# Kernel tuning notes

Measured on AMD Instinct MI355X. Metric: run time of the kernel, lower is better.

Reference implementation:

```python
import jax, jax.numpy as jnp
import numpy as np

# --- Mamba2Simple hyperparams (derived from init_kwargs) ---
D_MODEL = 2048
D_STATE = 128
HEADDIM = 64
EXPAND = 2
D_CONV = 4
NGROUPS = 1
CHUNK = 256
EPS = 1e-5
D_INNER = EXPAND * D_MODEL            # 4096
NHEADS = D_INNER // HEADDIM           # 64
CONV_DIM = D_INNER + 2 * NGROUPS * D_STATE          # 4352
D_IN_PROJ = 2 * D_INNER + 2 * NGROUPS * D_STATE + NHEADS  # 8512


def setup_inputs() -> dict:
    key = jax.random.key(0)
    ks = jax.random.split(key, 9)
    B, L = 2, 2048
    x = jax.random.normal(ks[0], (B, L, D_MODEL), jnp.float32)
    w_in = jax.random.normal(ks[1], (D_MODEL, D_IN_PROJ), jnp.float32) * (D_MODEL ** -0.5)
    conv_w = jax.random.normal(ks[2], (CONV_DIM, D_CONV), jnp.float32) * 0.2
    conv_b = jnp.zeros((CONV_DIM,), jnp.float32)
    dt_bias = jax.random.uniform(ks[3], (NHEADS,), jnp.float32, -4.0, -1.0)
    # A in [1, 16] per official init -> A_log = log(A)
    A_log = jnp.log(jax.random.uniform(ks[4], (NHEADS,), jnp.float32, 1.0, 16.0))
    D = jnp.ones((NHEADS,), jnp.float32)
    norm_w = jnp.ones((D_INNER,), jnp.float32)
    w_out = jax.random.normal(ks[5], (D_INNER, D_MODEL), jnp.float32) * (D_INNER ** -0.5)
    return {"x": x, "w_in": w_in, "conv_w": conv_w, "conv_b": conv_b,
            "dt_bias": dt_bias, "A_log": A_log, "D": D, "norm_w": norm_w, "w_out": w_out}


def _segsum(a):
    # a: (..., T) -> (..., T, T) with out[i, j] = sum_{k=j+1..i} a[k] for j<=i else -inf
    T = a.shape[-1]
    cs = jnp.cumsum(a, axis=-1)
    d = cs[..., :, None] - cs[..., None, :]
    mask = jnp.tril(jnp.ones((T, T), dtype=bool))
    return jnp.where(mask, d, -jnp.inf)


def _ssd(X, A, Bm, Cm):
    # X: (b, l, h, p) already multiplied by dt; A: (b, l, h) = dt*A_cont
    # Bm, Cm: (b, l, n)  (ngroups=1, broadcast over heads)
    b, l, h, p = X.shape
    n = Bm.shape[-1]
    c = l // CHUNK
    X = X.reshape(b, c, CHUNK, h, p)
    A = A.reshape(b, c, CHUNK, h).transpose(0, 3, 1, 2)      # (b, h, c, q)
    Bm = Bm.reshape(b, c, CHUNK, n)
    Cm = Cm.reshape(b, c, CHUNK, n)
    A_cs = jnp.cumsum(A, axis=-1)                             # (b, h, c, q)
    Lmat = jnp.exp(_segsum(A))                                # (b, h, c, q, q)
    # intra-chunk (diagonal block) output
    Y_diag = jnp.einsum("bcln,bcsn,bhcls,bcshp->bclhp", Cm, Bm, Lmat, X)
    # per-chunk final states
    decay_states = jnp.exp(A_cs[..., -1:] - A_cs)             # (b, h, c, q)
    states = jnp.einsum("bcln,bhcl,bclhp->bchpn", Bm, decay_states, X)
    # inter-chunk recurrence
    A_last = jnp.pad(A_cs[..., -1], ((0, 0), (0, 0), (1, 0)))  # (b, h, c+1)
    decay_chunk = jnp.exp(_segsum(A_last))                     # (b, h, c+1, c+1)
    states = jnp.concatenate([jnp.zeros_like(states[:, :1]), states], axis=1)
    states = jnp.einsum("bhzc,bchpn->bzhpn", decay_chunk, states)[:, :-1]
    # state -> output contribution
    Y_off = jnp.einsum("bchpn,bcln,bhcl->bclhp", states, Cm, jnp.exp(A_cs))
    return (Y_diag + Y_off).reshape(b, l, h, p)


def _mamba2(x, w_in, conv_w, conv_b, dt_bias, A_log, D, norm_w, w_out):
    B, L, _ = x.shape
    zxbcdt = jnp.einsum("bld,de->ble", x, w_in)               # (B, L, 8512)
    z = zxbcdt[..., :D_INNER]
    xBC = zxbcdt[..., D_INNER:D_INNER + CONV_DIM]
    dt = zxbcdt[..., D_INNER + CONV_DIM:]                      # (B, L, H)
    dt = jax.nn.softplus(dt + dt_bias)
    # causal depthwise conv1d + silu
    xp = jnp.pad(xBC, ((0, 0), (D_CONV - 1, 0), (0, 0)))
    acc = conv_b
    xBC = sum(conv_w[:, k] * xp[:, k:k + L, :] for k in range(D_CONV)) + conv_b
    xBC = jax.nn.silu(xBC)
    xh = xBC[..., :D_INNER].reshape(B, L, NHEADS, HEADDIM)
    Bm = xBC[..., D_INNER:D_INNER + NGROUPS * D_STATE]         # (B, L, N) since ngroups=1
    Cm = xBC[..., D_INNER + NGROUPS * D_STATE:]                # (B, L, N)
    A = -jnp.exp(A_log)                                        # (H,)
    y = _ssd(xh * dt[..., None], dt * A, Bm, Cm)               # (B, L, H, P)
    y = y + xh * D[None, None, :, None]                        # skip term
    y = y.reshape(B, L, D_INNER)
    # gated RMSNorm (norm_before_gate=False): normalize(y * silu(z)) * weight
    y = y * jax.nn.silu(z)
    y = y * jax.lax.rsqrt(jnp.mean(y * y, axis=-1, keepdims=True) + EPS) * norm_w
    return jnp.einsum("ble,ed->bld", y, w_out)


def reference(x, w_in, conv_w, conv_b, dt_bias, A_log, D, norm_w, w_out):
    return x + _mamba2(x, w_in, conv_w, conv_b, dt_bias, A_log, D, norm_w, w_out)
```

## Files before the change

### kernel.cpp

```cpp
#include <hip/hip_runtime.h>
#include <math.h>

#define DEV __device__ __forceinline__

typedef __attribute__((ext_vector_type(4))) float f32x4;
typedef __attribute__((ext_vector_type(4))) unsigned short u16x4;
typedef __attribute__((ext_vector_type(8))) unsigned short u16x8;
typedef __attribute__((ext_vector_type(8))) __bf16 bfv8;

DEV unsigned short f2bf(float f) {
  unsigned u = __builtin_bit_cast(unsigned, f);
  u = (u + 0x7FFFu + ((u >> 16) & 1u)) >> 16;
  return (unsigned short)u;
}
DEV float bf2f(unsigned short h) {
  unsigned u = ((unsigned)h) << 16;
  return __builtin_bit_cast(float, u);
}

DEV f32x4 mfma16(u16x8 a, u16x8 b, f32x4 c) {
  return __builtin_amdgcn_mfma_f32_16x16x32_bf16(
      __builtin_bit_cast(bfv8, a), __builtin_bit_cast(bfv8, b), c, 0, 0, 0);
}

DEV void gload_lds16(const unsigned short* g, unsigned short* s) {
  __builtin_amdgcn_global_load_lds(
      (const __attribute__((address_space(1))) void*)g,
      (__attribute__((address_space(3))) void*)s, 16, 0, 0);
}

template <int N>
DEV void vmcnt_wait() {
  if constexpr (N == 0) asm volatile("s_waitcnt vmcnt(0)" ::: "memory");
  else if constexpr (N == 2) asm volatile("s_waitcnt vmcnt(2)" ::: "memory");
  else if constexpr (N == 4) asm volatile("s_waitcnt vmcnt(4)" ::: "memory");
}

__global__ __launch_bounds__(512, 2) void gemm8_in(
    const unsigned short* __restrict__ A, const unsigned short* __restrict__ Bt,
    unsigned short* __restrict__ o_z, unsigned short* __restrict__ o_xbc,
    float* __restrict__ o_dt) {
  constexpr int K = 2048, NT = K / 64;
  __shared__ __align__(16) unsigned short As[2][256 * 64];
  __shared__ __align__(16) unsigned short Bs[2][256 * 64];
  const int tid = threadIdx.x;
  const int lane = tid & 63, w = tid >> 6;
  const int l16 = lane & 15, lq = lane >> 4;
  const int wr = w >> 1, wc = w & 1;
  const int nwg = gridDim.x * gridDim.y;
  int lin = blockIdx.y * gridDim.x + blockIdx.x;
  lin = (lin & 7) * (nwg >> 3) + (lin >> 3);
  const int m0 = (lin / gridDim.x) * 256, n0 = (lin % gridDim.x) * 256;
  const int srow = lane >> 3;
  const int schk = (lane & 7) ^ srow;
  const unsigned short* Ag = A + (size_t)(m0 + srow) * K + schk * 8;
  const unsigned short* Bg = Bt + (size_t)(n0 + srow) * K + schk * 8;
  const int px0 = lq ^ (l16 & 7);
  const int px1 = (4 + lq) ^ (l16 & 7);

  f32x4 acc[4][8] = {};

  auto stageA = [&](int p, int slot, int kt) {
    gload_lds16(Ag + (size_t)(slot * 64 + w * 8) * K + kt * 64,
                &As[p][(slot * 64 + w * 8) * 64]);
  };
  auto stageB = [&](int p, int slot, int kt) {
    gload_lds16(Bg + (size_t)(slot * 64 + w * 8) * K + kt * 64,
                &Bs[p][(slot * 64 + w * 8) * 64]);
  };
  auto rdA = [&](int p, int mf, int k2) -> u16x8 {
    const int row = wr * 64 + mf * 16 + l16;
    return *(const u16x8*)(&As[p][row * 64 + (k2 ? px1 : px0) * 8]);
  };
  auto rdB = [&](int p, int nf, int k2) -> u16x8 {
    const int row = wc * 128 + nf * 16 + l16;
    return *(const u16x8*)(&Bs[p][row * 64 + (k2 ? px1 : px0) * 8]);
  };

  stageA(0, 0, 0); stageA(0, 1, 0); stageA(0, 2, 0); stageA(0, 3, 0);
  stageB(0, 0, 0); stageB(0, 2, 0); stageB(0, 1, 0); stageB(0, 3, 0);
  vmcnt_wait<2>();
  __builtin_amdgcn_s_barrier();

  u16x8 a0[4], a1[4], b0[2], b1[2];
  for (int k = 0; k < NT; ++k) {
    const int p = k & 1, pn = p ^ 1;
    const bool st = (k + 1 < NT);
#pragma unroll
    for (int mf = 0; mf < 4; ++mf) { a0[mf] = rdA(p, mf, 0); a1[mf] = rdA(p, mf, 1); }
    b0[0] = rdB(p, 0, 0); b1[0] = rdB(p, 0, 1);
    b0[1] = rdB(p, 1, 0); b1[1] = rdB(p, 1, 1);
    if (st) { stageA(pn, 0, k + 1); stageA(pn, 1, k + 1); }
    __builtin_amdgcn_s_barrier();
    __builtin_amdgcn_s_setprio(1);
#pragma unroll
    for (int nf = 0; nf < 2; ++nf)
#pragma unroll
      for (int mf = 0; mf < 4; ++mf) {
        acc[mf][nf] = mfma16(a0[mf], b0[nf], acc[mf][nf]);
        acc[mf][nf] = mfma16(a1[mf], b1[nf], acc[mf][nf]);
      }
    __builtin_amdgcn_s_setprio(0);
    __builtin_amdgcn_s_barrier();
    b0[0] = rdB(p, 2, 0); b1[0] = rdB(p, 2, 1);
    b0[1] = rdB(p, 3, 0); b1[1] = rdB(p, 3, 1);
    if (st) { stageA(pn, 2, k + 1); stageA(pn, 3, k + 1); vmcnt_wait<4>(); }
    else vmcnt_wait<0>();
    __builtin_amdgcn_s_barrier();
    __builtin_amdgcn_s_setprio(1);
#pragma unroll
    for (int nf = 0; nf < 2; ++nf)
#pragma unroll
      for (int mf = 0; mf < 4; ++mf) {
        acc[mf][2 + nf] = mfma16(a0[mf], b0[nf], acc[mf][2 + nf]);
        acc[mf][2 + nf] = mfma16(a1[mf], b1[nf], acc[mf][2 + nf]);
      }
    __builtin_amdgcn_s_setprio(0);
    __builtin_amdgcn_s_barrier();
    b0[0] = rdB(p, 4, 0); b1[0] = rdB(p, 4, 1);
    b0[1] = rdB(p, 5, 0); b1[1] = rdB(p, 5, 1);
    if (st) { stageB(pn, 0, k + 1); stageB(pn, 2, k + 1); }
    __builtin_amdgcn_s_barrier();
    __builtin_amdgcn_s_setprio(1);
#pragma unroll
    for (int nf = 0; nf < 2; ++nf)
#pragma unroll
      for (int mf = 0; mf < 4; ++mf) {
        acc[mf][4 + nf] = mfma16(a0[mf], b0[nf], acc[mf][4 + nf]);
        acc[mf][4 + nf] = mfma16(a1[mf], b1[nf], acc[mf][4 + nf]);
      }
    __builtin_amdgcn_s_setprio(0);
    __builtin_amdgcn_s_barrier();
    b0[0] = rdB(p, 6, 0); b1[0] = rdB(p, 6, 1);
    b0[1] = rdB(p, 7, 0); b1[1] = rdB(p, 7, 1);
    if (st) { stageB(pn, 1, k + 1); stageB(pn, 3, k + 1); vmcnt_wait<2>(); }
    else vmcnt_wait<0>();
    __builtin_amdgcn_s_barrier();
    __builtin_amdgcn_s_setprio(1);
#pragma unroll
    for (int nf = 0; nf < 2; ++nf)
#pragma unroll
      for (int mf = 0; mf < 4; ++mf) {
        acc[mf][6 + nf] = mfma16(a0[mf], b0[nf], acc[mf][6 + nf]);
        acc[mf][6 + nf] = mfma16(a1[mf], b1[nf], acc[mf][6 + nf]);
      }
    __builtin_amdgcn_s_setprio(0);
    __builtin_amdgcn_s_barrier();
  }

#pragma unroll
  for (int mf = 0; mf < 4; ++mf) {
#pragma unroll
    for (int nf = 0; nf < 8; ++nf) {
      const int col = n0 + wc * 128 + nf * 16 + l16;
#pragma unroll
      for (int r = 0; r < 4; ++r) {
        const int row = m0 + wr * 64 + mf * 16 + lq * 4 + r;
        float v = acc[mf][nf][r];
        if (col < 4096) o_z[(size_t)row * 4096 + col] = f2bf(v);
        else if (col < 8448) o_xbc[(size_t)row * 4352 + (col - 4096)] = f2bf(v);
        else if (col < 8512) o_dt[(size_t)row * 64 + (col - 8448)] = v;
      }
    }
  }
}

__global__ __launch_bounds__(256, 3) void gemm_p(
    const unsigned short* __restrict__ A, const unsigned short* __restrict__ Bt,
    int K, float* __restrict__ o_c, const float* __restrict__ resid) {
  __shared__ __align__(16) unsigned short As[3][128 * 32];
  __shared__ __align__(16) unsigned short Bs[3][128 * 32];
  const int tid = threadIdx.x;
  const int lane = tid & 63, w = tid >> 6;
  const int l16 = lane & 15, lq = lane >> 4;
  const int wr = w >> 1, wc = w & 1;
  const int nwg = gridDim.x * gridDim.y;
  int lin = blockIdx.y * gridDim.x + blockIdx.x;
  lin = (lin & 7) * (nwg >> 3) + (lin >> 3);
  const int m0 = (lin / gridDim.x) * 128, n0 = (lin % gridDim.x) * 128;
  const int lrow = lane >> 2;
  const int gq = (lane & 3) ^ ((lrow >> 1) & 3);
  const int cq = lq ^ ((l16 >> 1) & 3);

  const unsigned short* Ag = A + (size_t)(m0 + lrow) * K + gq * 8;
  const unsigned short* Bg = Bt + (size_t)(n0 + lrow) * K + gq * 8;

  f32x4 acc[4][4] = {};

  auto stage = [&](int bi, int kt) {
#pragma unroll
    for (int i = 0; i < 2; ++i) {
      const int rb = (w + i * 4) * 16;
      gload_lds16(Ag + (size_t)rb * K + kt * 32, &As[bi][rb * 32]);
    }
#pragma unroll
    for (int i = 0; i < 2; ++i) {
      const int rb = (w + i * 4) * 16;
      gload_lds16(Bg + (size_t)rb * K + kt * 32, &Bs[bi][rb * 32]);
    }
  };

  const int nt = K / 32;
  stage(0, 0);
  stage(1, 1);

  for (int k = 0; k < nt; ++k) {
    const int cb = k % 3;
    if (k < nt - 1) vmcnt_wait<4>();
    else vmcnt_wait<0>();
    __builtin_amdgcn_s_barrier();
    if (k + 2 < nt) stage((k + 2) % 3, k + 2);

    u16x8 af[4], bf[4];
#pragma unroll
    for (int mf = 0; mf < 4; ++mf)
      af[mf] = *(const u16x8*)(&As[cb][(wr * 64 + mf * 16 + l16) * 32 + cq * 8]);
#pragma unroll
    for (int nf = 0; nf < 4; ++nf)
      bf[nf] = *(const u16x8*)(&Bs[cb][(wc * 64 + nf * 16 + l16) * 32 + cq * 8]);

    __builtin_amdgcn_s_setprio(1);
#pragma unroll
    for (int mf = 0; mf < 4; ++mf)
#pragma unroll
      for (int nf = 0; nf < 4; ++nf)
        acc[mf][nf] = mfma16(af[mf], bf[nf], acc[mf][nf]);
    __builtin_amdgcn_s_setprio(0);
  }

#pragma unroll
  for (int mf = 0; mf < 4; ++mf) {
#pragma unroll
    for (int nf = 0; nf < 4; ++nf) {
      const int col = n0 + wc * 64 + nf * 16 + l16;
#pragma unroll
      for (int r = 0; r < 4; ++r) {
        const int row = m0 + wr * 64 + mf * 16 + lq * 4 + r;
        size_t idx = (size_t)row * 2048 + col;
        o_c[idx] = acc[mf][nf][r] + resid[idx];
      }
    }
  }
}

__global__ __launch_bounds__(256) void convert_bf16(
    const float* __restrict__ in, unsigned short* __restrict__ out) {
  const size_t i = ((size_t)blockIdx.x * 256 + threadIdx.x) * 8;
  f32x4 a = *(const f32x4*)(in + i);
  f32x4 b = *(const f32x4*)(in + i + 4);
  u16x8 o;
#pragma unroll
  for (int j = 0; j < 4; ++j) { o[j] = f2bf(a[j]); o[j + 4] = f2bf(b[j]); }
  *(u16x8*)(out + i) = o;
}

__global__ __launch_bounds__(256) void transpose_conv(
    const float* __restrict__ in, unsigned short* __restrict__ out, int R,
    int C) {
  __shared__ __align__(16) unsigned short T[64][72];
  const int c0 = blockIdx.x * 64, r0 = blockIdx.y * 64;
  const int tid = threadIdx.x;
#pragma unroll
  for (int it = 0; it < 4; ++it) {
    int r = it * 16 + (tid >> 4);
    int c = (tid & 15) * 4;
    f32x4 v = {0.f, 0.f, 0.f, 0.f};
    if (c0 + c < C) v = *(const f32x4*)(in + (size_t)(r0 + r) * C + c0 + c);
#pragma unroll
    for (int j = 0; j < 4; ++j) T[c + j][r] = f2bf(v[j]);
  }
  __syncthreads();
  const int nr = tid >> 2, kc = (tid & 3) * 16;
  u16x8 a = *(const u16x8*)(&T[nr][kc]);
  u16x8 b = *(const u16x8*)(&T[nr][kc + 8]);
  unsigned short* o = out + (size_t)(c0 + nr) * R + r0 + kc;
  *(u16x8*)o = a;
  *(u16x8*)(o + 8) = b;
}

__global__ __launch_bounds__(256) void conv_kernel(
    const unsigned short* __restrict__ raw, const float* __restrict__ cw,
    const float* __restrict__ cb, unsigned short* __restrict__ xbc) {
  const int ch4 = blockIdx.x * 256 + threadIdx.x;
  if (ch4 >= 1088) return;
  const int ch = ch4 * 4;
  const int r0 = blockIdx.y * 4;
  const int l0 = r0 & 2047;
  f32x4 w0 = *(const f32x4*)(cw + ch * 4);
  f32x4 w1 = *(const f32x4*)(cw + ch * 4 + 4);
  f32x4 w2 = *(const f32x4*)(cw + ch * 4 + 8);
  f32x4 w3 = *(const f32x4*)(cw + ch * 4 + 12);
  f32x4 bias = *(const f32x4*)(cb + ch);
  f32x4 v[7];
#pragma unroll
  for (int i = 0; i < 7; ++i) {
    if (l0 - 3 + i >= 0) {
      u16x4 h = *(const u16x4*)(raw + (size_t)(r0 - 3 + i) * 4352 + ch);
      v[i] = (f32x4){bf2f(h[0]), bf2f(h[1]), bf2f(h[2]), bf2f(h[3])};
    } else {
      v[i] = (f32x4){0.f, 0.f, 0.f, 0.f};
    }
  }
#pragma unroll
  for (int j = 0; j < 4; ++j) {
    f32x4 acc = bias;
#pragma unroll
    for (int k = 0; k < 4; ++k) {
      acc[0] += w0[k] * v[j + k][0];
      acc[1] += w1[k] * v[j + k][1];
      acc[2] += w2[k] * v[j + k][2];
      acc[3] += w3[k] * v[j + k][3];
    }
    u16x4 o;
#pragma unroll
    for (int q = 0; q < 4; ++q) {
      float s = acc[q] / (1.0f + __expf(-acc[q]));
      o[q] = f2bf(s);
    }
    *(u16x4*)(xbc + (size_t)(r0 + j) * 4352 + ch) = o;
  }
}

__global__ __launch_bounds__(256) void dt_kernel(
    float* __restrict__ dtb, const float* __restrict__ dt_bias,
    const float* __restrict__ A_log, float* __restrict__ Acs) {
  __shared__ float ws[4];
  const int blk = blockIdx.x;
  const int c = blk & 7, h = (blk >> 3) & 63, b = blk >> 9;
  const int t = threadIdx.x;
  const int lane = t & 63, w = t >> 6;
  const int row = b * 2048 + c * 256 + t;
  float xv = dtb[(size_t)row * 64 + h] + dt_bias[h];
  float dt = (xv > 20.0f) ? xv : log1pf(__expf(xv));
  dtb[(size_t)row * 64 + h] = dt;
  float s = dt * (-__expf(A_log[h]));
#pragma unroll
  for (int off = 1; off < 64; off <<= 1) {
    float v = __shfl_up(s, off, 64);
    if (lane >= off) s += v;
  }
  if (lane == 63) ws[w] = s;
  __syncthreads();
  float base = 0.0f;
#pragma unroll
  for (int i = 0; i < 4; ++i)
    if (i < w) base += ws[i];
  Acs[((size_t)((b * 64 + h) * 8 + c)) * 256 + t] = s + base;
}

__global__ __launch_bounds__(256) void g_kernel(
    const unsigned short* __restrict__ xbc, float* __restrict__ G) {
  const int bc = blockIdx.y;
  const int i0 = (blockIdx.x >> 2) * 64, j0 = (blockIdx.x & 3) * 64;
  const int tid = threadIdx.x;
  const int lane = tid & 63, w = tid >> 6;
  const int l16 = lane & 15, lq = lane >> 4;
  const unsigned short* base = xbc + (size_t)bc * 256 * 4352;
  f32x4 acc[4] = {};
#pragma unroll
  for (int ks = 0; ks < 4; ++ks) {
    int nb = ks * 32 + lq * 8;
    u16x8 af = *(const u16x8*)(base + (size_t)(i0 + w * 16 + l16) * 4352 + 4224 + nb);
#pragma unroll
    for (int jf = 0; jf < 4; ++jf) {
      u16x8 bb = *(const u16x8*)(base + (size_t)(j0 + jf * 16 + l16) * 4352 + 4096 + nb);
      acc[jf] = mfma16(af, bb, acc[jf]);
    }
  }
  float* Gt = G + (size_t)bc * 65536;
#pragma unroll
  for (int jf = 0; jf < 4; ++jf)
#pragma unroll
    for (int r = 0; r < 4; ++r)
      Gt[(i0 + w * 16 + lq * 4 + r) * 256 + j0 + jf * 16 + l16] = acc[jf][r];
}

__global__ __launch_bounds__(512) void ssd_states(
    const unsigned short* __restrict__ xbc, const float* __restrict__ dtb,
    const float* __restrict__ Acs, unsigned short* __restrict__ statesb) {
  __shared__ __align__(16) unsigned short Xt[64 * 264];
  __shared__ __align__(16) unsigned short BmT[128 * 72];
  __shared__ float As_s[256];
  const int h = blockIdx.x, c = blockIdx.y, b = blockIdx.z;
  const int tid = threadIdx.x;
  const int lane = tid & 63, w = tid >> 6;
  const int l16 = lane & 15, lq = lane >> 4;
  const int row0 = b * 2048 + c * 256;

  if (tid < 256) As_s[tid] = Acs[((size_t)((b * 64 + h) * 8 + c)) * 256 + tid];
#pragma unroll
  for (int it = 0; it < 2; ++it) {
    int pb = tid & 15;
    int tb = it * 32 + (tid >> 4);
    float rr[4][4];
#pragma unroll
    for (int i = 0; i < 4; ++i) {
      int row = row0 + tb * 4 + i;
      u16x4 v = *(const u16x4*)(xbc + (size_t)row * 4352 + h * 64 + pb * 4);
      float dtv = dtb[(size_t)row * 64 + h];
#pragma unroll
      for (int j = 0; j < 4; ++j) rr[i][j] = bf2f(v[j]) * dtv;
    }
#pragma unroll
    for (int j = 0; j < 4; ++j) {
      u16x4 hh = {f2bf(rr[0][j]), f2bf(rr[1][j]), f2bf(rr[2][j]), f2bf(rr[3][j])};
      *(u16x4*)(&Xt[(pb * 4 + j) * 264 + tb * 4]) = hh;
    }
  }
  __syncthreads();

  f32x4 accS[4] = {};
  const float Alast = As_s[255];
  for (int part = 0; part < 4; ++part) {
    if (part) __syncthreads();
    {
      int nb = tid & 31;
      int tb = tid >> 5;
      float rr[4][4];
#pragma unroll
      for (int i = 0; i < 4; ++i) {
        int t = part * 64 + tb * 4 + i;
        int row = row0 + t;
        float dec = __expf(Alast - As_s[t]);
        u16x4 v = *(const u16x4*)(xbc + (size_t)row * 4352 + 4096 + nb * 4);
#pragma unroll
        for (int j = 0; j < 4; ++j) rr[i][j] = bf2f(v[j]) * dec;
      }
#pragma unroll
      for (int j = 0; j < 4; ++j) {
        u16x4 hh = {f2bf(rr[0][j]), f2bf(rr[1][j]), f2bf(rr[2][j]), f2bf(rr[3][j])};
        *(u16x4*)(&BmT[(nb * 4 + j) * 72 + tb * 4]) = hh;
      }
    }
    __syncthreads();
#pragma unroll
    for (int ks = 0; ks < 2; ++ks) {
      int toff = ks * 32 + lq * 8;
      u16x8 af = *(const u16x8*)(&BmT[(w * 16 + l16) * 72 + toff]);
#pragma unroll
      for (int pf = 0; pf < 4; ++pf) {
        u16x8 bfr = *(const u16x8*)(&Xt[(pf * 16 + l16) * 264 + part * 64 + toff]);
        accS[pf] = mfma16(af, bfr, accS[pf]);
      }
    }
  }
  unsigned short* Sp = statesb + (size_t)((b * 8 + c) * 64 + h) * 8192;
#pragma unroll
  for (int pf = 0; pf < 4; ++pf) {
    u16x4 hh = {f2bf(accS[pf][0]), f2bf(accS[pf][1]), f2bf(accS[pf][2]),
                f2bf(accS[pf][3])};
    *(u16x4*)(&Sp[(pf * 16 + l16) * 128 + w * 16 + lq * 4]) = hh;
  }
}

__global__ __launch_bounds__(256) void scan_states(
    const unsigned short* __restrict__ statesb, const float* __restrict__ Acs,
    unsigned short* __restrict__ prefix) {
  const int h = blockIdx.x, b = blockIdx.y;
  const int tid = threadIdx.x;
  const int p = tid >> 2, nq = (tid & 3) * 32;
  float S[32];
#pragma unroll
  for (int i = 0; i < 32; ++i) S[i] = 0.0f;
  for (int cc = 0; cc < 8; ++cc) {
    size_t base = (size_t)((b * 8 + cc) * 64 + h) * 8192 + p * 128 + nq;
#pragma unroll
    for (int j = 0; j < 4; ++j) {
      u16x8 hh;
#pragma unroll
      for (int k = 0; k < 8; ++k) hh[k] = f2bf(S[j * 8 + k]);
      *(u16x8*)(prefix + base + j * 8) = hh;
    }
    float eAl = __expf(Acs[((size_t)((b * 64 + h) * 8 + cc)) * 256 + 255]);
#pragma unroll
    for (int j = 0; j < 4; ++j) {
      u16x8 v = *(const u16x8*)(statesb + base + j * 8);
#pragma unroll
      for (int k = 0; k < 8; ++k) S[j * 8 + k] = eAl * S[j * 8 + k] + bf2f(v[k]);
    }
  }
}

__global__ __launch_bounds__(512) void ssd_main(
    const unsigned short* __restrict__ xbc, const float* __restrict__ dtb,
    const float* __restrict__ Acs, const float* __restrict__ G,
    const unsigned short* __restrict__ prefix, const float* __restrict__ Dv,
    unsigned short* __restrict__ y) {
  __shared__ __align__(16) unsigned short Xt[64 * 264];
  __shared__ float As_s[256];
  const int h = blockIdx.x, c = blockIdx.y, b = blockIdx.z;
  const int tid = threadIdx.x;
  const int lane = tid & 63, w = tid >> 6;
  const int l16 = lane & 15, lq = lane >> 4;
  const int row0 = b * 2048 + c * 256;

  if (tid < 256) As_s[tid] = Acs[((size_t)((b * 64 + h) * 8 + c)) * 256 + tid];
#pragma unroll
  for (int it = 0; it < 2; ++it) {
    int pb = tid & 15;
    int tb = it * 32 + (tid >> 4);
    float rr[4][4];
#pragma unroll
    for (int i = 0; i < 4; ++i) {
      int row = row0 + tb * 4 + i;
      u16x4 v = *(const u16x4*)(xbc + (size_t)row * 4352 + h * 64 + pb * 4);
      float dtv = dtb[(size_t)row * 64 + h];
#pragma unroll
      for (int j = 0; j < 4; ++j) rr[i][j] = bf2f(v[j]) * dtv;
    }
#pragma unroll
    for (int j = 0; j < 4; ++j) {
      u16x4 hh = {f2bf(rr[0][j]), f2bf(rr[1][j]), f2bf(rr[2][j]), f2bf(rr[3][j])};
      *(u16x4*)(&Xt[(pb * 4 + j) * 264 + tb * 4]) = hh;
    }
  }
  __syncthreads();

  f32x4 acc[2][4] = {};
  const float* Gt = G + (size_t)(b * 8 + c) * 65536;
  for (int ks = 0; ks < 8; ++ks) {
    const int tb = ks * 32 + lq * 8;
    u16x8 bfr[4];
#pragma unroll
    for (int pf = 0; pf < 4; ++pf)
      bfr[pf] = *(const u16x8*)(&Xt[(pf * 16 + l16) * 264 + tb]);
#pragma unroll
    for (int mf = 0; mf < 2; ++mf) {
      const int i = w * 32 + mf * 16 + l16;
      const float ai = As_s[i];
      const float* gp = Gt + i * 256 + tb;
      f32x4 g0 = *(const f32x4*)gp;
      f32x4 g1 = *(const f32x4*)(gp + 4);
      u16x8 af;
#pragma unroll
      for (int jj = 0; jj < 8; ++jj) {
        int j = tb + jj;
        float g = (jj < 4) ? g0[jj] : g1[jj - 4];
        float v = (i >= j) ? g * __expf(ai - As_s[j]) : 0.0f;
        af[jj] = f2bf(v);
      }
#pragma unroll
      for (int pf = 0; pf < 4; ++pf)
        acc[mf][pf] = mfma16(af, bfr[pf], acc[mf][pf]);
    }
  }
  const unsigned short* Pf = prefix + (size_t)((b * 8 + c) * 64 + h) * 8192;
  for (int ks = 0; ks < 4; ++ks) {
    const int nb = ks * 32 + lq * 8;
    u16x8 bfr[4];
#pragma unroll
    for (int pf = 0; pf < 4; ++pf)
      bfr[pf] = *(const u16x8*)(Pf + (size_t)(pf * 16 + l16) * 128 + nb);
#pragma unroll
    for (int mf = 0; mf < 2; ++mf) {
      const int i = w * 32 + mf * 16 + l16;
      const float eAi = __expf(As_s[i]);
      u16x8 cv = *(const u16x8*)(xbc + (size_t)(row0 + i) * 4352 + 4224 + nb);
      u16x8 af;
#pragma unroll
      for (int jj = 0; jj < 8; ++jj) af[jj] = f2bf(bf2f(cv[jj]) * eAi);
#pragma unroll
      for (int pf = 0; pf < 4; ++pf)
        acc[mf][pf] = mfma16(af, bfr[pf], acc[mf][pf]);
    }
  }
  const float Dh = Dv[h];
#pragma unroll
  for (int mf = 0; mf < 2; ++mf) {
#pragma unroll
    for (int r = 0; r < 4; ++r) {
      int t = w * 32 + mf * 16 + lq * 4 + r;
      size_t row = (size_t)(row0 + t);
#pragma unroll
      for (int pf = 0; pf < 4; ++pf) {
        int p = pf * 16 + l16;
        float xh = bf2f(xbc[row * 4352 + h * 64 + p]);
        y[row * 4096 + h * 64 + p] = f2bf(acc[mf][pf][r] + Dh * xh);
      }
    }
  }
}

__global__ __launch_bounds__(256) void norm_kernel(
    unsigned short* __restrict__ y, const unsigned short* __restrict__ zbf,
    const float* __restrict__ nw) {
  const int row = blockIdx.x, tid = threadIdx.x;
  unsigned short* yr = y + (size_t)row * 4096;
  const unsigned short* zr = zbf + (size_t)row * 4096;
  float vals[16];
  float ss = 0.0f;
#pragma unroll
  for (int i = 0; i < 2; ++i) {
    int cb = i * 2048 + tid * 8;
    u16x8 yv = *(const u16x8*)(yr + cb);
    u16x8 zv = *(const u16x8*)(zr + cb);
#pragma unroll
    for (int j = 0; j < 8; ++j) {
      float z = bf2f(zv[j]);
      float g = bf2f(yv[j]) * (z / (1.0f + __expf(-z)));
      vals[i * 8 + j] = g;
      ss += g * g;
    }
  }
#pragma unroll
  for (int off = 32; off > 0; off >>= 1) ss += __shfl_xor(ss, off, 64);
  __shared__ float red[4];
  if ((tid & 63) == 0) red[tid >> 6] = ss;
  __syncthreads();
  float tot = red[0] + red[1] + red[2] + red[3];
  float rr = rsqrtf(tot * (1.0f / 4096.0f) + 1e-5f);
#pragma unroll
  for (int i = 0; i < 2; ++i) {
    int cb = i * 2048 + tid * 8;
    f32x4 w0 = *(const f32x4*)(nw + cb);
    f32x4 w1 = *(const f32x4*)(nw + cb + 4);
    u16x8 o;
#pragma unroll
    for (int j = 0; j < 8; ++j) {
      float wv = (j < 4) ? w0[j] : w1[j - 4];
      o[j] = f2bf(vals[i * 8 + j] * rr * wv);
    }
    *(u16x8*)(yr + cb) = o;
  }
}

extern "C" void kernel_launch(void* const* d_in, const int* in_sizes, int n_in,
                              void* d_out, int out_size, void* d_ws,
                              size_t ws_size, hipStream_t stream) {
  const float* x = (const float*)d_in[0];
  const float* w_in = (const float*)d_in[1];
  const float* conv_w = (const float*)d_in[2];
  const float* conv_b = (const float*)d_in[3];
  const float* dt_bias = (const float*)d_in[4];
  const float* A_log = (const float*)d_in[5];
  const float* Dvec = (const float*)d_in[6];
  const float* norm_w = (const float*)d_in[7];
  const float* w_out = (const float*)d_in[8];
  float* out = (float*)d_out;

  char* w = (char*)d_ws;
  unsigned short* zbf = (unsigned short*)(w + 0);
  unsigned short* xbc = (unsigned short*)(w + 33554432);
  unsigned short* xbcraw = (unsigned short*)(w + 69206016);
  float* dtb = (float*)(w + 104857600);
  float* Acs = (float*)(w + 105906176);
  float* G = (float*)(w + 106954752);
  unsigned short* statesb = (unsigned short*)(w + 111149056);
  unsigned short* y = (unsigned short*)(w + 127926272);
  unsigned short* xbf = (unsigned short*)(w + 111149056);
  unsigned short* w_inT = (unsigned short*)(w + 33554432);
  unsigned short* w_outT = (unsigned short*)(w + 33554432);
  unsigned short* prefix = xbcraw;

  convert_bf16<<<dim3(4096), 256, 0, stream>>>(x, xbf);
  transpose_conv<<<dim3(136, 32), 256, 0, stream>>>(w_in, w_inT, 2048, 8512);
  gemm8_in<<<dim3(34, 16), 512, 0, stream>>>(xbf, w_inT, zbf, xbcraw, dtb);
  conv_kernel<<<dim3(5, 1024), 256, 0, stream>>>(xbcraw, conv_w, conv_b, xbc);
  dt_kernel<<<dim3(1024), 256, 0, stream>>>(dtb, dt_bias, A_log, Acs);
  g_kernel<<<dim3(16, 16), 256, 0, stream>>>(xbc, G);
  ssd_states<<<dim3(64, 8, 2), 512, 0, stream>>>(xbc, dtb, Acs, statesb);
  scan_states<<<dim3(64, 2), 256, 0, stream>>>(statesb, Acs, prefix);
  ssd_main<<<dim3(64, 8, 2), 512, 0, stream>>>(xbc, dtb, Acs, G, prefix, Dvec, y);
  transpose_conv<<<dim3(32, 64), 256, 0, stream>>>(w_out, w_outT, 4096, 2048);
  norm_kernel<<<dim3(4096), 256, 0, stream>>>(y, zbf, norm_w);
  gemm_p<<<dim3(16, 32), 256, 0, stream>>>(y, w_outT, 4096, out, x);
}
```

Before: 466.7 us.

## Restructure in-proj GEMM warp tiling to 2x4 with B loaded two steps ahead

Changes the in-projection GEMM warp layout from 4x2 (64x128 per warp) to 2x4 (128x64 per warp), so each warp keeps B fragments in registers across four sub-phases and streams A fragments instead. The staging schedule is reworked so the next A tile goes into the alternate buffer while the B tile for step t+2 is prefetched into the current slot once its fragments are in registers. The aim is fewer LDS reads for B and a deeper pipeline for B loads. The risks are higher register pressure and a subtle reuse of the LDS buffer, with correctness depending on the barrier placement.

```diff
diff --git a/kernel.cpp b/kernel.cpp
--- a/kernel.cpp
+++ b/kernel.cpp
@@ -32,8 +32,8 @@
 template <int N>
 DEV void vmcnt_wait() {
   if constexpr (N == 0) asm volatile("s_waitcnt vmcnt(0)" ::: "memory");
-  else if constexpr (N == 2) asm volatile("s_waitcnt vmcnt(2)" ::: "memory");
   else if constexpr (N == 4) asm volatile("s_waitcnt vmcnt(4)" ::: "memory");
+  else if constexpr (N == 8) asm volatile("s_waitcnt vmcnt(8)" ::: "memory");
 }
 
 __global__ __launch_bounds__(512, 2) void gemm8_in(
@@ -46,7 +46,7 @@
   const int tid = threadIdx.x;
   const int lane = tid & 63, w = tid >> 6;
   const int l16 = lane & 15, lq = lane >> 4;
-  const int wr = w >> 1, wc = w & 1;
+  const int wr = w >> 2, wc = w & 3;
   const int nwg = gridDim.x * gridDim.y;
   int lin = blockIdx.y * gridDim.x + blockIdx.x;
   lin = (lin & 7) * (nwg >> 3) + (lin >> 3);
@@ -58,105 +58,87 @@
   const int px0 = lq ^ (l16 & 7);
   const int px1 = (4 + lq) ^ (l16 & 7);
 
-  f32x4 acc[4][8] = {};
-
-  auto stageA = [&](int p, int slot, int kt) {
-    gload_lds16(Ag + (size_t)(slot * 64 + w * 8) * K + kt * 64,
-                &As[p][(slot * 64 + w * 8) * 64]);
+  f32x4 acc[8][4] = {};
+
+  auto stA = [&](int sl, int h, int kt) {
+#pragma unroll
+    for (int i = 0; i < 2; ++i) {
+      const int rb = h * 128 + i * 64 + w * 8;
+      gload_lds16(Ag + (size_t)rb * K + kt * 64, &As[sl][rb * 64]);
+    }
   };
-  auto stageB = [&](int p, int slot, int kt) {
-    gload_lds16(Bg + (size_t)(slot * 64 + w * 8) * K + kt * 64,
-                &Bs[p][(slot * 64 + w * 8) * 64]);
+  auto stB = [&](int sl, int h, int kt) {
+#pragma unroll
+    for (int i = 0; i < 2; ++i) {
+      const int rb = h * 128 + i * 64 + w * 8;
+      gload_lds16(Bg + (size_t)rb * K + kt * 64, &Bs[sl][rb * 64]);
+    }
   };
-  auto rdA = [&](int p, int mf, int k2) -> u16x8 {
-    const int row = wr * 64 + mf * 16 + l16;
-    return *(const u16x8*)(&As[p][row * 64 + (k2 ? px1 : px0) * 8]);
+  auto rdA = [&](int sl, int row, int k2) -> u16x8 {
+    return *(const u16x8*)(&As[sl][row * 64 + (k2 ? px1 : px0) * 8]);
   };
-  auto rdB = [&](int p, int nf, int k2) -> u16x8 {
-    const int row = wc * 128 + nf * 16 + l16;
-    return *(const u16x8*)(&Bs[p][row * 64 + (k2 ? px1 : px0) * 8]);
+  auto rdB = [&](int sl, int row, int k2) -> u16x8 {
+    return *(const u16x8*)(&Bs[sl][row * 64 + (k2 ? px1 : px0) * 8]);
   };
 
-  stageA(0, 0, 0); stageA(0, 1, 0); stageA(0, 2, 0); stageA(0, 3, 0);
-  stageB(0, 0, 0); stageB(0, 2, 0); stageB(0, 1, 0); stageB(0, 3, 0);
-  vmcnt_wait<2>();
+  stA(0, 0, 0); stA(0, 1, 0);
+  stB(0, 0, 0); stB(0, 1, 0);
+  stB(1, 0, 1); stB(1, 1, 1);
+  vmcnt_wait<4>();
   __builtin_amdgcn_s_barrier();
 
-  u16x8 a0[4], a1[4], b0[2], b1[2];
-  for (int k = 0; k < NT; ++k) {
-    const int p = k & 1, pn = p ^ 1;
-    const bool st = (k + 1 < NT);
-#pragma unroll
-    for (int mf = 0; mf < 4; ++mf) { a0[mf] = rdA(p, mf, 0); a1[mf] = rdA(p, mf, 1); }
-    b0[0] = rdB(p, 0, 0); b1[0] = rdB(p, 0, 1);
-    b0[1] = rdB(p, 1, 0); b1[1] = rdB(p, 1, 1);
-    if (st) { stageA(pn, 0, k + 1); stageA(pn, 1, k + 1); }
-    __builtin_amdgcn_s_barrier();
-    __builtin_amdgcn_s_setprio(1);
-#pragma unroll
-    for (int nf = 0; nf < 2; ++nf)
-#pragma unroll
-      for (int mf = 0; mf < 4; ++mf) {
-        acc[mf][nf] = mfma16(a0[mf], b0[nf], acc[mf][nf]);
-        acc[mf][nf] = mfma16(a1[mf], b1[nf], acc[mf][nf]);
-      }
-    __builtin_amdgcn_s_setprio(0);
-    __builtin_amdgcn_s_barrier();
-    b0[0] = rdB(p, 2, 0); b1[0] = rdB(p, 2, 1);
-    b0[1] = rdB(p, 3, 0); b1[1] = rdB(p, 3, 1);
-    if (st) { stageA(pn, 2, k + 1); stageA(pn, 3, k + 1); vmcnt_wait<4>(); }
-    else vmcnt_wait<0>();
-    __builtin_amdgcn_s_barrier();
-    __builtin_amdgcn_s_setprio(1);
-#pragma unroll
-    for (int nf = 0; nf < 2; ++nf)
-#pragma unroll
-      for (int mf = 0; mf < 4; ++mf) {
-        acc[mf][2 + nf] = mfma16(a0[mf], b0[nf], acc[mf][2 + nf]);
-        acc[mf][2 + nf] = mfma16(a1[mf], b1[nf], acc[mf][2 + nf]);
-      }
-    __builtin_amdgcn_s_setprio(0);
-    __builtin_amdgcn_s_barrier();
-    b0[0] = rdB(p, 4, 0); b1[0] = rdB(p, 4, 1);
-    b0[1] = rdB(p, 5, 0); b1[1] = rdB(p, 5, 1);
-    if (st) { stageB(pn, 0, k + 1); stageB(pn, 2, k + 1); }
-    __builtin_amdgcn_s_barrier();
-    __builtin_amdgcn_s_setprio(1);
-#pragma unroll
-    for (int nf = 0; nf < 2; ++nf)
-#pragma unroll
-      for (int mf = 0; mf < 4; ++mf) {
-        acc[mf][4 + nf] = mfma16(a0[mf], b0[nf], acc[mf][4 + nf]);
-        acc[mf][4 + nf] = mfma16(a1[mf], b1[nf], acc[mf][4 + nf]);
-      }
-    __builtin_amdgcn_s_setprio(0);
-    __builtin_amdgcn_s_barrier();
-    b0[0] = rdB(p, 6, 0); b1[0] = rdB(p, 6, 1);
-    b0[1] = rdB(p, 7, 0); b1[1] = rdB(p, 7, 1);
-    if (st) { stageB(pn, 1, k + 1); stageB(pn, 3, k + 1); vmcnt_wait<2>(); }
-    else vmcnt_wait<0>();
-    __builtin_amdgcn_s_barrier();
-    __builtin_amdgcn_s_setprio(1);
-#pragma unroll
-    for (int nf = 0; nf < 2; ++nf)
-#pragma unroll
-      for (int mf = 0; mf < 4; ++mf) {
-        acc[mf][6 + nf] = mfma16(a0[mf], b0[nf], acc[mf][6 + nf]);
-        acc[mf][6 + nf] = mfma16(a1[mf], b1[nf], acc[mf][6 + nf]);
-      }
-    __builtin_amdgcn_s_setprio(0);
-    __builtin_amdgcn_s_barrier();
-  }
-
-#pragma unroll
-  for (int mf = 0; mf < 4; ++mf) {
-#pragma unroll
-    for (int nf = 0; nf < 8; ++nf) {
-      const int col = n0 + wc * 128 + nf * 16 + l16;
+  u16x8 br[4][2];
+  for (int t = 0; t < NT; ++t) {
+    const int sl = t & 1, so = sl ^ 1;
+    const bool hasA = (t + 1 < NT), hasB = (t + 2 < NT);
+#pragma unroll
+    for (int p = 0; p < 4; ++p) {
+      u16x8 ar[2][2];
+#pragma unroll
+      for (int mf = 0; mf < 2; ++mf) {
+        const int row = wr * 128 + p * 32 + mf * 16 + l16;
+        ar[mf][0] = rdA(sl, row, 0);
+        ar[mf][1] = rdA(sl, row, 1);
+      }
+      if (p == 0) {
+#pragma unroll
+        for (int nf = 0; nf < 4; ++nf) {
+          const int row = wc * 64 + nf * 16 + l16;
+          br[nf][0] = rdB(sl, row, 0);
+          br[nf][1] = rdB(sl, row, 1);
+        }
+      }
+      if (p == 0) { if (hasA) stA(so, 0, t + 1); }
+      else if (p == 1) { if (hasA) stA(so, 1, t + 1); }
+      else if (p == 2) { if (hasB) stB(sl, 0, t + 2); }
+      else {
+        if (hasB) stB(sl, 1, t + 2);
+        if (t < NT - 2) vmcnt_wait<4>();
+        else vmcnt_wait<0>();
+      }
+      __builtin_amdgcn_s_barrier();
+      __builtin_amdgcn_s_setprio(1);
+#pragma unroll
+      for (int nf = 0; nf < 4; ++nf)
+#pragma unroll
+        for (int mf = 0; mf < 2; ++mf) {
+          acc[p * 2 + mf][nf] = mfma16(ar[mf][0], br[nf][0], acc[p * 2 + mf][nf]);
+          acc[p * 2 + mf][nf] = mfma16(ar[mf][1], br[nf][1], acc[p * 2 + mf][nf]);
+        }
+      __builtin_amdgcn_s_setprio(0);
+      __builtin_amdgcn_s_barrier();
+    }
+  }
+
+#pragma unroll
+  for (int q = 0; q < 8; ++q) {
+#pragma unroll
+    for (int nf = 0; nf < 4; ++nf) {
+      const int col = n0 + wc * 64 + nf * 16 + l16;
 #pragma unroll
       for (int r = 0; r < 4; ++r) {
-        const int row = m0 + wr * 64 + mf * 16 + lq * 4 + r;
-        float v = acc[mf][nf][r];
+        const int row = m0 + wr * 128 + (q >> 1) * 32 + (q & 1) * 16 + lq * 4 + r;
+        float v = acc[q][nf][r];
         if (col < 4096) o_z[(size_t)row * 4096 + col] = f2bf(v);
         else if (col < 8448) o_xbc[(size_t)row * 4352 + (col - 4096)] = f2bf(v);
         else if (col < 8512) o_dt[(size_t)row * 64 + (col - 8448)] = v;
```

After: 524.9 us. 1.12x slower.
